# Optimization experiments

Hardware: AMD Instinct MI355X
Metric: run time of the kernel (lower is better)

Reference implementation:

```python
import jax, jax.numpy as jnp
import numpy as np

BS, SEQ, VOCAB, EMS, NHID, ML = 32, 512, 5000, 256, 512, 16
TEMP = 0.9
GAMMA = 0.0  # self.gamma is a fixed zero Variable in the original


def setup_inputs() -> dict:
    key = jax.random.key(0)
    ks = jax.random.split(key, 10)
    nm = SEQ // ML
    inputs = jax.random.randint(ks[0], (BS, SEQ), 0, VOCAB, dtype=jnp.int32)
    measure_steps = jax.random.randint(ks[1], (ML, BS, nm), 0, VOCAB, dtype=jnp.int32)
    measure_weights = jax.random.normal(ks[2], (BS, nm, nm), dtype=jnp.float32)
    h0 = jnp.zeros((BS, NHID), jnp.float32)
    c0 = jnp.zeros((BS, NHID), jnp.float32)
    initrange = 0.1
    emb = jax.random.uniform(ks[3], (VOCAB, EMS), minval=-initrange, maxval=initrange)
    k = 1.0 / np.sqrt(NHID).astype(np.float32)
    W_ih = jax.random.uniform(ks[4], (4 * NHID, EMS), minval=-k, maxval=k)
    W_hh = jax.random.uniform(ks[5], (4 * NHID, NHID), minval=-k, maxval=k)
    b_ih = jax.random.uniform(ks[6], (4 * NHID,), minval=-k, maxval=k)
    b_hh = jax.random.uniform(ks[7], (4 * NHID,), minval=-k, maxval=k)
    W_dec = jax.random.uniform(ks[8], (VOCAB, NHID), minval=-initrange, maxval=initrange)
    b_dec = jnp.zeros((VOCAB,), jnp.float32)
    return dict(inputs=inputs, h0=h0, c0=c0, measure_weights=measure_weights,
                measure_steps=measure_steps, emb=emb, W_ih=W_ih, W_hh=W_hh,
                b_ih=b_ih, b_hh=b_hh, W_dec=W_dec, b_dec=b_dec, measure_length=ML)


def _forward(h0, c0, mw, emb, W_ih, W_hh, b_ih, b_hh, W_dec, b_dec,
             inputs, msteps, measure_length):
    bs, seq = inputs.shape
    nm = seq // measure_length
    # attention over previous measures: softmax over j < m (causal-masked)
    mask = (jnp.arange(nm)[None, :] < jnp.arange(nm)[:, None]).astype(mw.dtype)  # [m, j]
    logits = jnp.where(mask[None] > 0, mw / TEMP, -1e9)
    sm = jax.nn.softmax(logits, axis=-1) * mask[None]  # [bs, m, j]
    prev_embs = emb[msteps]  # [ML, bs, nm, E]
    # lookback embedding for (measure m, step s): sum_j sm[b,m,j] * emb[steps[s,b,j]]
    lb = jnp.einsum('bmj,sbje->msbe', sm, prev_embs)  # [nm, ML, bs, E]
    lb_seq = lb.reshape(seq, bs, -1)  # time-major: t = m*ML + s
    # per-step bmm decode against embedding table: [bs, seq, V]
    lookback = jnp.einsum('tbe,ve->btv', lb_seq, emb)
    # original zeros lookback for timesteps with int(i/num_measures)==0, i.e. i < nm
    tmask = (jnp.arange(seq) >= nm)[None, :, None]
    lookback = jnp.where(tmask, lookback, jnp.zeros((), lookback.dtype))

    x = emb[inputs]  # [bs, seq, E] (single channel -> concat is identity)

    def cell(carry, xt):
        h, c = carry
        g = xt @ W_ih.T + b_ih + h @ W_hh.T + b_hh
        i, f, gg, o = jnp.split(g, 4, axis=-1)
        c2 = jax.nn.sigmoid(f) * c + jax.nn.sigmoid(i) * jnp.tanh(gg)
        h2 = jax.nn.sigmoid(o) * jnp.tanh(c2)
        return (h2, c2), h2

    (hT, cT), hs = jax.lax.scan(cell, (h0, c0), jnp.swapaxes(x, 0, 1))
    out = jnp.swapaxes(hs, 0, 1)  # [bs, seq, nhid]
    decoded = out @ W_dec.T + b_dec  # [bs, seq, V]
    dec = (1.0 - GAMMA) * decoded + GAMMA * lookback
    return dec, hT, cT


def reference(inputs, h0, c0, measure_weights, measure_steps, emb,
              W_ih, W_hh, b_ih, b_hh, W_dec, b_dec, measure_length):
    return _forward(h0, c0, measure_weights, emb, W_ih, W_hh, b_ih, b_hh,
                    W_dec, b_dec, inputs, measure_steps, measure_length)
```

## Files before the change

### kernel.cpp

```cpp
#include <hip/hip_runtime.h>
#include <cstdint>
#include <cstddef>

#define BS     32
#define SEQ    512
#define VOCAB  5000
#define EMS    256
#define NHID   512
#define GH     2048
#define NWG    32
#define SLICE  16
#define VPAD   5120

#define WS_FLAGS 0
#define WS_BIAS  1024
#define WS_WIH   (WS_BIAS + GH*4)
#define WS_WHH   (WS_WIH + GH*EMS*2)
#define WS_WDH   (WS_WHH + GH*NHID*2)
#define WS_WDL   (WS_WDH + VPAD*NHID*2)
#define WS_X     (WS_WDL + VPAD*NHID*2)
#define WS_HHI   (WS_X + SEQ*BS*EMS*2)
#define WS_HLO   (WS_HHI + BS*SEQ*NHID*2)
#define WS_HBUF  (WS_HLO + BS*SEQ*NHID*2)
#define WS_END   (WS_HBUF + 2*BS*NHID*2)

typedef float f32x4 __attribute__((ext_vector_type(4)));
typedef __bf16 bf16x8 __attribute__((ext_vector_type(8)));

static __device__ __forceinline__ uint16_t f2bf(float x) {
  uint32_t u = __builtin_bit_cast(uint32_t, x);
  u += 0x7FFFu + ((u >> 16) & 1u);
  return (uint16_t)(u >> 16);
}
static __device__ __forceinline__ float bf2f(uint16_t b) {
  return __builtin_bit_cast(float, (uint32_t)b << 16);
}
static __device__ __forceinline__ float sigf(float x) { return 1.0f / (1.0f + __expf(-x)); }
static __device__ __forceinline__ float tanhf_fast(float x) {
  return 1.0f - 2.0f / (__expf(2.0f * x) + 1.0f);
}
static __device__ __forceinline__ f32x4 mfma16(uint4 a, uint4 b, f32x4 c) {
  return __builtin_amdgcn_mfma_f32_16x16x32_bf16(
      __builtin_bit_cast(bf16x8, a), __builtin_bit_cast(bf16x8, b), c, 0, 0, 0);
}
static __device__ __forceinline__ void glds16(const void* g, void* l) {
  __builtin_amdgcn_global_load_lds((__attribute__((address_space(1))) void*)g,
                                   (__attribute__((address_space(3))) void*)l,
                                   16, 0, 0);
}
static __device__ __forceinline__ void coh_store_u32(uint32_t* p, uint32_t v) {
  __hip_atomic_store(p, v, __ATOMIC_RELAXED, __HIP_MEMORY_SCOPE_AGENT);
}

__global__ __launch_bounds__(256) void prep_kernel(
    const int* __restrict__ inputs, const float* __restrict__ h0,
    const float* __restrict__ emb, const float* __restrict__ Wih,
    const float* __restrict__ Whh, const float* __restrict__ bih,
    const float* __restrict__ bhh, const float* __restrict__ Wd,
    char* __restrict__ ws) {
  int gid = blockIdx.x * 256 + threadIdx.x;
  int gsz = gridDim.x * 256;
  uint16_t* wX  = (uint16_t*)(ws + WS_X);
  uint16_t* wIH = (uint16_t*)(ws + WS_WIH);
  uint16_t* wHH = (uint16_t*)(ws + WS_WHH);
  uint16_t* wDH = (uint16_t*)(ws + WS_WDH);
  uint16_t* wDL = (uint16_t*)(ws + WS_WDL);
  float*    bias = (float*)(ws + WS_BIAS);
  uint16_t* hb  = (uint16_t*)(ws + WS_HBUF);
  if (gid < 32) ((uint32_t*)(ws + WS_FLAGS))[gid] = 0u;
  for (int i = gid; i < SEQ*BS*EMS; i += gsz) {
    int e = i & (EMS-1), b = (i >> 8) & (BS-1), t = i >> 13;
    wX[i] = f2bf(emb[(size_t)inputs[b*SEQ + t] * EMS + e]);
  }
  for (int i = gid; i < GH*EMS; i += gsz)  wIH[i] = f2bf(Wih[i]);
  for (int i = gid; i < GH*NHID; i += gsz) wHH[i] = f2bf(Whh[i]);
  for (int i = gid; i < VPAD*NHID; i += gsz) {
    int row = i >> 9;
    uint16_t hi = 0, lo = 0;
    if (row < VOCAB) {
      float x = Wd[i];
      hi = f2bf(x);
      lo = f2bf(x - bf2f(hi));
    }
    wDH[i] = hi; wDL[i] = lo;
  }
  for (int i = gid; i < GH; i += gsz) bias[i] = bih[i] + bhh[i];
  for (int i = gid; i < BS*NHID; i += gsz) hb[i] = f2bf(h0[i]);
}

template <int KSTEPS, int NPASS>
__global__ __launch_bounds__(256) void gemm_kernel(
    const uint16_t* __restrict__ A0, const uint16_t* __restrict__ A1,
    const uint16_t* __restrict__ A2, const uint16_t* __restrict__ B0,
    const uint16_t* __restrict__ B1, const uint16_t* __restrict__ B2,
    const float* __restrict__ bias, float* __restrict__ out,
    int Nvalid, int ldout) {
  constexpr int K = KSTEPS * 32;
  constexpr int TOT = KSTEPS * NPASS;
  __shared__ __align__(16) char lds[4][8192];
  const int tid = threadIdx.x;
  const int lane = tid & 63, w = tid >> 6;
  const int m0 = blockIdx.y * 128, n0 = blockIdx.x * 128;
  const uint16_t* As[3] = {A0, A1, A2};
  const uint16_t* Bs[3] = {B0, B1, B2};
  const int wbase = (tid & ~63);

  auto stage = [&](int buf, int s) {
    const int p = s / KSTEPS, kk = s % KSTEPS;
    const uint16_t* A = As[p];
    const uint16_t* B = Bs[p];
    char* dA = &lds[buf*2][0];
    char* dB = &lds[buf*2+1][0];
#pragma unroll
    for (int c = 0; c < 2; ++c) {
      int idx = c*256 + tid;
      int row = idx >> 2, col = (idx & 3) * 8;
      glds16(A + (size_t)(m0 + row) * K + kk*32 + col, dA + (c*256 + wbase)*16);
      glds16(B + (size_t)(n0 + row) * K + kk*32 + col, dB + (c*256 + wbase)*16);
    }
  };

  const f32x4 zero = {0.f, 0.f, 0.f, 0.f};
  f32x4 acc[4][4];
#pragma unroll
  for (int i = 0; i < 4; ++i)
#pragma unroll
    for (int j = 0; j < 4; ++j) acc[i][j] = zero;

  const int mq = (w >> 1) * 64, nq = (w & 1) * 64;
  stage(0, 0);
  for (int s = 0; s < TOT; ++s) {
    __syncthreads();
    if (s + 1 < TOT) stage((s + 1) & 1, s + 1);
    const char* cA = &lds[(s & 1)*2][0];
    const char* cB = &lds[(s & 1)*2+1][0];
    uint4 a[4], b[4];
#pragma unroll
    for (int i = 0; i < 4; ++i) {
      a[i] = *(const uint4*)(cA + (mq + i*16 + (lane & 15))*64 + (lane >> 4)*16);
      b[i] = *(const uint4*)(cB + (nq + i*16 + (lane & 15))*64 + (lane >> 4)*16);
    }
#pragma unroll
    for (int i = 0; i < 4; ++i)
#pragma unroll
      for (int j = 0; j < 4; ++j) acc[i][j] = mfma16(a[i], b[j], acc[i][j]);
  }
#pragma unroll
  for (int j = 0; j < 4; ++j) {
    int V = n0 + nq + j*16 + (lane & 15);
    if (V >= Nvalid) continue;
    float bv = bias[V];
#pragma unroll
    for (int i = 0; i < 4; ++i) {
      int Rb = m0 + mq + i*16 + (lane >> 4)*4;
#pragma unroll
      for (int r = 0; r < 4; ++r)
        out[(size_t)(Rb + r) * ldout + V] = acc[i][j][r] + bv;
    }
  }
}

__global__ __launch_bounds__(256, 1) void scan_kernel(
    const float* __restrict__ Gin, char* __restrict__ ws,
    const float* __restrict__ c0, float* __restrict__ outT) {
  __shared__ __align__(16) char sW[64*1024];
  __shared__ __align__(16) char sH[32*1024];
  __shared__ float sG[4*BS*SLICE];
  const uint16_t* wHH = (const uint16_t*)(ws + WS_WHH);
  uint16_t* hbuf = (uint16_t*)(ws + WS_HBUF);
  uint16_t* Hhi  = (uint16_t*)(ws + WS_HHI);
  uint16_t* Hlo  = (uint16_t*)(ws + WS_HLO);
  uint32_t* flags = (uint32_t*)(ws + WS_FLAGS);
  const int tid = threadIdx.x, wg = blockIdx.x;
  const int lane = tid & 63, w = tid >> 6;
  const int mw = w >> 1, nw = w & 1;

  for (int c = tid; c < 4096; c += 256) {
    int row = c >> 6;
    int kb = (c & 63) * 16;
    int G = row >> 4, dl = row & 15;
    uint4 v = *(const uint4*)(wHH + (size_t)(G*NHID + wg*SLICE + dl) * NHID + kb/2);
    *(uint4*)(sW + row*1024 + (kb ^ ((row & 7) << 4))) = v;
  }
  const int bq = tid >> 3, dq = (tid & 7) * 2;
  float c_0 = c0[bq*NHID + wg*SLICE + dq];
  float c_1 = c0[bq*NHID + wg*SLICE + dq + 1];
  const int arow = mw*16 + (lane & 15);
  const int brow0 = (2*nw)*16 + (lane & 15);
  const int brow1 = brow0 + 16;
  const int kb0 = (lane >> 4) * 16;

  float ga0[4], ga1[4], gb0[4], gb1[4];
  {
    const float* grow = Gin + wg*SLICE + (lane & 15);
#pragma unroll
    for (int r = 0; r < 4; ++r) {
      int b = mw*16 + (lane >> 4)*4 + r;
      ga0[r] = grow[(size_t)b*GH + (2*nw+0)*NHID];
      ga1[r] = grow[(size_t)b*GH + (2*nw+1)*NHID];
    }
  }
  __syncthreads();

  for (int t = 0; t < SEQ; ++t) {
    if (t > 0) {
      const uint32_t tgt = (uint32_t)t;
      const int fl = lane & 31;
      while (true) {
        uint32_t v = __hip_atomic_load(flags + fl, __ATOMIC_RELAXED, __HIP_MEMORY_SCOPE_AGENT);
        if (__all((int)(v >= tgt))) break;
      }
    }

    if (t + 1 < SEQ) {
      const float* grow = Gin + (size_t)(t+1)*(BS*GH) + wg*SLICE + (lane & 15);
#pragma unroll
      for (int r = 0; r < 4; ++r) {
        int b = mw*16 + (lane >> 4)*4 + r;
        gb0[r] = grow[(size_t)b*GH + (2*nw+0)*NHID];
        gb1[r] = grow[(size_t)b*GH + (2*nw+1)*NHID];
      }
    }

    {
      const char* hsrc = (const char*)(hbuf + (t & 1) * (BS*NHID));
      const char* pb = hsrc + tid * 16;
      uint4 v0, v1, v2, v3, v4, v5, v6, v7;
      asm volatile("global_load_dwordx4 %0, %1, off sc0 sc1" : "=v"(v0) : "v"(pb));
      asm volatile("global_load_dwordx4 %0, %1, off sc0 sc1" : "=v"(v1) : "v"(pb + 4096));
      asm volatile("global_load_dwordx4 %0, %1, off sc0 sc1" : "=v"(v2) : "v"(pb + 8192));
      asm volatile("global_load_dwordx4 %0, %1, off sc0 sc1" : "=v"(v3) : "v"(pb + 12288));
      asm volatile("global_load_dwordx4 %0, %1, off sc0 sc1" : "=v"(v4) : "v"(pb + 16384));
      asm volatile("global_load_dwordx4 %0, %1, off sc0 sc1" : "=v"(v5) : "v"(pb + 20480));
      asm volatile("global_load_dwordx4 %0, %1, off sc0 sc1" : "=v"(v6) : "v"(pb + 24576));
      asm volatile("global_load_dwordx4 %0, %1, off sc0 sc1" : "=v"(v7) : "v"(pb + 28672));
      asm volatile("s_waitcnt vmcnt(0)" ::: "memory");
      __builtin_amdgcn_sched_barrier(0);
      const int kb = (tid & 63) * 16;
      const int ww = tid >> 6;
#define STW(J, VJ) *(uint4*)(sH + ((J)*4 + ww)*1024 + (kb ^ ((((J)&1)*4 + ww) << 4))) = VJ;
      STW(0, v0) STW(1, v1) STW(2, v2) STW(3, v3)
      STW(4, v4) STW(5, v5) STW(6, v6) STW(7, v7)
#undef STW
    }
    __syncthreads();

    f32x4 acc0, acc1;
#pragma unroll
    for (int r = 0; r < 4; ++r) { acc0[r] = ga0[r]; acc1[r] = ga1[r]; }
#pragma unroll
    for (int kt = 0; kt < 16; ++kt) {
      int kb = kt*64 + kb0;
      uint4 av = *(const uint4*)(sH + arow*1024 + (kb ^ ((arow & 7) << 4)));
      uint4 b0 = *(const uint4*)(sW + brow0*1024 + (kb ^ ((brow0 & 7) << 4)));
      uint4 b1 = *(const uint4*)(sW + brow1*1024 + (kb ^ ((brow1 & 7) << 4)));
      acc0 = mfma16(av, b0, acc0);
      acc1 = mfma16(av, b1, acc1);
    }
#pragma unroll
    for (int r = 0; r < 4; ++r) {
      int b = mw*16 + (lane >> 4)*4 + r;
      sG[((2*nw+0)*BS + b)*SLICE + (lane & 15)] = acc0[r];
      sG[((2*nw+1)*BS + b)*SLICE + (lane & 15)] = acc1[r];
    }
#pragma unroll
    for (int r = 0; r < 4; ++r) { ga0[r] = gb0[r]; ga1[r] = gb1[r]; }
    __syncthreads();

    float gi0 = sG[(0*BS + bq)*SLICE + dq], gi1 = sG[(0*BS + bq)*SLICE + dq + 1];
    float gf0 = sG[(1*BS + bq)*SLICE + dq], gf1 = sG[(1*BS + bq)*SLICE + dq + 1];
    float gg0 = sG[(2*BS + bq)*SLICE + dq], gg1 = sG[(2*BS + bq)*SLICE + dq + 1];
    float go0 = sG[(3*BS + bq)*SLICE + dq], go1 = sG[(3*BS + bq)*SLICE + dq + 1];
    c_0 = sigf(gf0)*c_0 + sigf(gi0)*tanhf_fast(gg0);
    c_1 = sigf(gf1)*c_1 + sigf(gi1)*tanhf_fast(gg1);
    float h_0 = sigf(go0)*tanhf_fast(c_0);
    float h_1 = sigf(go1)*tanhf_fast(c_1);

    uint16_t hh0 = f2bf(h_0), hh1 = f2bf(h_1);
    uint32_t hp = (uint32_t)hh0 | ((uint32_t)hh1 << 16);
    coh_store_u32((uint32_t*)(hbuf + ((t+1) & 1)*(BS*NHID)) +
                      ((bq*NHID + wg*SLICE + dq) >> 1), hp);
    size_t hoff = ((size_t)bq*SEQ + t)*NHID + wg*SLICE + dq;
    *(uint32_t*)(Hhi + hoff) = hp;
    uint32_t lp = (uint32_t)f2bf(h_0 - bf2f(hh0)) | ((uint32_t)f2bf(h_1 - bf2f(hh1)) << 16);
    *(uint32_t*)(Hlo + hoff) = lp;
    if (t == SEQ-1) {
      outT[bq*NHID + wg*SLICE + dq]     = h_0;
      outT[bq*NHID + wg*SLICE + dq + 1] = h_1;
      outT[BS*NHID + bq*NHID + wg*SLICE + dq]     = c_0;
      outT[BS*NHID + bq*NHID + wg*SLICE + dq + 1] = c_1;
    }

    __syncthreads();
    if (tid == 0)
      __hip_atomic_store(flags + wg, (uint32_t)(t + 1), __ATOMIC_RELAXED,
                         __HIP_MEMORY_SCOPE_AGENT);
  }
}

extern "C" void kernel_launch(void* const* d_in, const int* in_sizes, int n_in,
                              void* d_out, int out_size, void* d_ws, size_t ws_size,
                              hipStream_t stream) {
  (void)in_sizes; (void)n_in; (void)out_size; (void)ws_size;
  const int*   inputs = (const int*)  d_in[0];
  const float* h0     = (const float*)d_in[1];
  const float* c0     = (const float*)d_in[2];
  const float* emb    = (const float*)d_in[5];
  const float* Wih    = (const float*)d_in[6];
  const float* Whh    = (const float*)d_in[7];
  const float* bih    = (const float*)d_in[8];
  const float* bhh    = (const float*)d_in[9];
  const float* Wdec   = (const float*)d_in[10];
  const float* bdec   = (const float*)d_in[11];
  char* ws   = (char*)d_ws;
  float* out = (float*)d_out;
  float* Gin  = out;
  float* outT = out + (size_t)BS*SEQ*VOCAB;

  prep_kernel<<<512, 256, 0, stream>>>(inputs, h0, emb, Wih, Whh, bih, bhh, Wdec, ws);
  gemm_kernel<8,1><<<dim3(GH/128, (BS*SEQ)/128), 256, 0, stream>>>(
      (const uint16_t*)(ws + WS_X), (const uint16_t*)(ws + WS_X), (const uint16_t*)(ws + WS_X),
      (const uint16_t*)(ws + WS_WIH), (const uint16_t*)(ws + WS_WIH), (const uint16_t*)(ws + WS_WIH),
      (const float*)(ws + WS_BIAS), Gin, GH, GH);
  scan_kernel<<<NWG, 256, 0, stream>>>(Gin, ws, c0, outT);
  gemm_kernel<16,3><<<dim3(VPAD/128, (BS*SEQ)/128), 256, 0, stream>>>(
      (const uint16_t*)(ws + WS_HHI), (const uint16_t*)(ws + WS_HHI), (const uint16_t*)(ws + WS_HLO),
      (const uint16_t*)(ws + WS_WDH), (const uint16_t*)(ws + WS_WDL), (const uint16_t*)(ws + WS_WDH),
      bdec, out, VOCAB, VOCAB);
}
```

Before: 2.056 ms.

## Replace per-block flag barrier with step-tagged hidden-state words in scan

```diff
diff --git a/kernel.cpp b/kernel.cpp
--- a/kernel.cpp
+++ b/kernel.cpp
@@ -12,7 +12,6 @@
 #define SLICE  16
 #define VPAD   5120
 
-#define WS_FLAGS 0
 #define WS_BIAS  1024
 #define WS_WIH   (WS_BIAS + GH*4)
 #define WS_WHH   (WS_WIH + GH*EMS*2)
@@ -21,8 +20,8 @@
 #define WS_X     (WS_WDL + VPAD*NHID*2)
 #define WS_HHI   (WS_X + SEQ*BS*EMS*2)
 #define WS_HLO   (WS_HHI + BS*SEQ*NHID*2)
-#define WS_HBUF  (WS_HLO + BS*SEQ*NHID*2)
-#define WS_END   (WS_HBUF + 2*BS*NHID*2)
+#define WS_TAG   (WS_HLO + BS*SEQ*NHID*2)
+#define WS_END   (WS_TAG + 2*8192*8)
 
 typedef float f32x4 __attribute__((ext_vector_type(4)));
 typedef __bf16 bf16x8 __attribute__((ext_vector_type(8)));
@@ -47,9 +46,6 @@
   __builtin_amdgcn_global_load_lds((__attribute__((address_space(1))) void*)g,
                                    (__attribute__((address_space(3))) void*)l,
                                    16, 0, 0);
-}
-static __device__ __forceinline__ void coh_store_u32(uint32_t* p, uint32_t v) {
-  __hip_atomic_store(p, v, __ATOMIC_RELAXED, __HIP_MEMORY_SCOPE_AGENT);
 }
 
 __global__ __launch_bounds__(256) void prep_kernel(
@@ -66,8 +62,7 @@
   uint16_t* wDH = (uint16_t*)(ws + WS_WDH);
   uint16_t* wDL = (uint16_t*)(ws + WS_WDL);
   float*    bias = (float*)(ws + WS_BIAS);
-  uint16_t* hb  = (uint16_t*)(ws + WS_HBUF);
-  if (gid < 32) ((uint32_t*)(ws + WS_FLAGS))[gid] = 0u;
+  unsigned long long* Tg = (unsigned long long*)(ws + WS_TAG);
   for (int i = gid; i < SEQ*BS*EMS; i += gsz) {
     int e = i & (EMS-1), b = (i >> 8) & (BS-1), t = i >> 13;
     wX[i] = f2bf(emb[(size_t)inputs[b*SEQ + t] * EMS + e]);
@@ -85,7 +80,14 @@
     wDH[i] = hi; wDL[i] = lo;
   }
   for (int i = gid; i < GH; i += gsz) bias[i] = bih[i] + bhh[i];
-  for (int i = gid; i < BS*NHID; i += gsz) hb[i] = f2bf(h0[i]);
+  for (int u = gid; u < 8192; u += gsz) {
+    int tc = u >> 5, j = u & 31;
+    int b = tc & 31, d = (tc >> 5) * 64 + j * 2;
+    uint32_t pay = (uint32_t)f2bf(h0[b*NHID + d]) |
+                   ((uint32_t)f2bf(h0[b*NHID + d + 1]) << 16);
+    Tg[u] = (unsigned long long)pay;
+    Tg[8192 + u] = 0xFFFFFFFF00000000ull;
+  }
 }
 
 template <int KSTEPS, int NPASS>
@@ -167,10 +169,9 @@
   __shared__ __align__(16) char sH[32*1024];
   __shared__ float sG[4*BS*SLICE];
   const uint16_t* wHH = (const uint16_t*)(ws + WS_WHH);
-  uint16_t* hbuf = (uint16_t*)(ws + WS_HBUF);
+  unsigned long long* Tg = (unsigned long long*)(ws + WS_TAG);
   uint16_t* Hhi  = (uint16_t*)(ws + WS_HHI);
   uint16_t* Hlo  = (uint16_t*)(ws + WS_HLO);
-  uint32_t* flags = (uint32_t*)(ws + WS_FLAGS);
   const int tid = threadIdx.x, wg = blockIdx.x;
   const int lane = tid & 63, w = tid >> 6;
   const int mw = w >> 1, nw = w & 1;
@@ -189,6 +190,8 @@
   const int brow0 = (2*nw)*16 + (lane & 15);
   const int brow1 = brow0 + 16;
   const int kb0 = (lane >> 4) * 16;
+  const int dmy = wg*SLICE + dq;
+  const int uidx = ((dmy >> 6) * 32 + bq) * 32 + ((dmy & 63) >> 1);
 
   float ga0[4], ga1[4], gb0[4], gb1[4];
   {
@@ -203,15 +206,6 @@
   __syncthreads();
 
   for (int t = 0; t < SEQ; ++t) {
-    if (t > 0) {
-      const uint32_t tgt = (uint32_t)t;
-      const int fl = lane & 31;
-      while (true) {
-        uint32_t v = __hip_atomic_load(flags + fl, __ATOMIC_RELAXED, __HIP_MEMORY_SCOPE_AGENT);
-        if (__all((int)(v >= tgt))) break;
-      }
-    }
-
     if (t + 1 < SEQ) {
       const float* grow = Gin + (size_t)(t+1)*(BS*GH) + wg*SLICE + (lane & 15);
 #pragma unroll
@@ -223,24 +217,47 @@
     }
 
     {
-      const char* hsrc = (const char*)(hbuf + (t & 1) * (BS*NHID));
-      const char* pb = hsrc + tid * 16;
-      uint4 v0, v1, v2, v3, v4, v5, v6, v7;
-      asm volatile("global_load_dwordx4 %0, %1, off sc0 sc1" : "=v"(v0) : "v"(pb));
-      asm volatile("global_load_dwordx4 %0, %1, off sc0 sc1" : "=v"(v1) : "v"(pb + 4096));
-      asm volatile("global_load_dwordx4 %0, %1, off sc0 sc1" : "=v"(v2) : "v"(pb + 8192));
-      asm volatile("global_load_dwordx4 %0, %1, off sc0 sc1" : "=v"(v3) : "v"(pb + 12288));
-      asm volatile("global_load_dwordx4 %0, %1, off sc0 sc1" : "=v"(v4) : "v"(pb + 16384));
-      asm volatile("global_load_dwordx4 %0, %1, off sc0 sc1" : "=v"(v5) : "v"(pb + 20480));
-      asm volatile("global_load_dwordx4 %0, %1, off sc0 sc1" : "=v"(v6) : "v"(pb + 24576));
-      asm volatile("global_load_dwordx4 %0, %1, off sc0 sc1" : "=v"(v7) : "v"(pb + 28672));
-      asm volatile("s_waitcnt vmcnt(0)" ::: "memory");
-      __builtin_amdgcn_sched_barrier(0);
-      const int kb = (tid & 63) * 16;
-      const int ww = tid >> 6;
-#define STW(J, VJ) *(uint4*)(sH + ((J)*4 + ww)*1024 + (kb ^ ((((J)&1)*4 + ww) << 4))) = VJ;
-      STW(0, v0) STW(1, v1) STW(2, v2) STW(3, v3)
-      STW(4, v4) STW(5, v5) STW(6, v6) STW(7, v7)
+      const char* tb = (const char*)(Tg + (size_t)(t & 1) * 8192) + tid * 256;
+      const uint32_t tg = (uint32_t)t;
+#define QD(J) uint2 q##J;
+      QD(0) QD(1) QD(2) QD(3) QD(4) QD(5) QD(6) QD(7)
+      QD(8) QD(9) QD(10) QD(11) QD(12) QD(13) QD(14) QD(15)
+      QD(16) QD(17) QD(18) QD(19) QD(20) QD(21) QD(22) QD(23)
+      QD(24) QD(25) QD(26) QD(27) QD(28) QD(29) QD(30) QD(31)
+#undef QD
+      uint32_t tries = 0;
+      for (;;) {
+#define PQ(J, OFF) asm volatile("global_load_dwordx2 %0, %1, off offset:" OFF " sc0 sc1" \
+                                : "=v"(q##J) : "v"(tb));
+        PQ(0,"0")    PQ(1,"8")    PQ(2,"16")   PQ(3,"24")
+        PQ(4,"32")   PQ(5,"40")   PQ(6,"48")   PQ(7,"56")
+        PQ(8,"64")   PQ(9,"72")   PQ(10,"80")  PQ(11,"88")
+        PQ(12,"96")  PQ(13,"104") PQ(14,"112") PQ(15,"120")
+        PQ(16,"128") PQ(17,"136") PQ(18,"144") PQ(19,"152")
+        PQ(20,"160") PQ(21,"168") PQ(22,"176") PQ(23,"184")
+        PQ(24,"192") PQ(25,"200") PQ(26,"208") PQ(27,"216")
+        PQ(28,"224") PQ(29,"232") PQ(30,"240") PQ(31,"248")
+#undef PQ
+        asm volatile("s_waitcnt vmcnt(0)" ::: "memory");
+        __builtin_amdgcn_sched_barrier(0);
+        uint32_t bad =
+            (q0.y^tg)|(q1.y^tg)|(q2.y^tg)|(q3.y^tg)|(q4.y^tg)|(q5.y^tg)|(q6.y^tg)|(q7.y^tg)|
+            (q8.y^tg)|(q9.y^tg)|(q10.y^tg)|(q11.y^tg)|(q12.y^tg)|(q13.y^tg)|(q14.y^tg)|(q15.y^tg)|
+            (q16.y^tg)|(q17.y^tg)|(q18.y^tg)|(q19.y^tg)|(q20.y^tg)|(q21.y^tg)|(q22.y^tg)|(q23.y^tg)|
+            (q24.y^tg)|(q25.y^tg)|(q26.y^tg)|(q27.y^tg)|(q28.y^tg)|(q29.y^tg)|(q30.y^tg)|(q31.y^tg);
+        if (bad == 0) break;
+        if (++tries > (1u << 20)) break;
+      }
+      char* dst = sH + (tid & 31) * 1024;
+      const int cb = (tid >> 5) * 128;
+      const int sw = (tid & 7) << 4;
+      uint4 wv;
+#define STW(K, A, B, C, D) wv.x = A.x; wv.y = B.x; wv.z = C.x; wv.w = D.x; \
+      *(uint4*)(dst + ((cb + (K)*16) ^ sw)) = wv;
+      STW(0, q0, q1, q2, q3)     STW(1, q4, q5, q6, q7)
+      STW(2, q8, q9, q10, q11)   STW(3, q12, q13, q14, q15)
+      STW(4, q16, q17, q18, q19) STW(5, q20, q21, q22, q23)
+      STW(6, q24, q25, q26, q27) STW(7, q28, q29, q30, q31)
 #undef STW
     }
     __syncthreads();
@@ -278,8 +295,9 @@
 
     uint16_t hh0 = f2bf(h_0), hh1 = f2bf(h_1);
     uint32_t hp = (uint32_t)hh0 | ((uint32_t)hh1 << 16);
-    coh_store_u32((uint32_t*)(hbuf + ((t+1) & 1)*(BS*NHID)) +
-                      ((bq*NHID + wg*SLICE + dq) >> 1), hp);
+    __hip_atomic_store(Tg + (size_t)((t + 1) & 1) * 8192 + uidx,
+                       ((unsigned long long)(uint32_t)(t + 1) << 32) | (unsigned long long)hp,
+                       __ATOMIC_RELAXED, __HIP_MEMORY_SCOPE_AGENT);
     size_t hoff = ((size_t)bq*SEQ + t)*NHID + wg*SLICE + dq;
     *(uint32_t*)(Hhi + hoff) = hp;
     uint32_t lp = (uint32_t)f2bf(h_0 - bf2f(hh0)) | ((uint32_t)f2bf(h_1 - bf2f(hh1)) << 16);
@@ -290,11 +308,6 @@
       outT[BS*NHID + bq*NHID + wg*SLICE + dq]     = c_0;
       outT[BS*NHID + bq*NHID + wg*SLICE + dq + 1] = c_1;
     }
-
-    __syncthreads();
-    if (tid == 0)
-      __hip_atomic_store(flags + wg, (uint32_t)(t + 1), __ATOMIC_RELAXED,
-                         __HIP_MEMORY_SCOPE_AGENT);
   }
 }
 
```

Result: slower. 4.009 ms (+95.0%).

## Fuse input projection, LSTM scan and decoder GEMM into one persistent kernel

Applied to the files above, without the earlier changes.

```diff
diff --git a/kernel.cpp b/kernel.cpp
--- a/kernel.cpp
+++ b/kernel.cpp
@@ -11,9 +11,12 @@
 #define NWG    32
 #define SLICE  16
 #define VPAD   5120
+#define NBLK   256
+#define NDEC   (NBLK - NWG)
+#define NTILE  ((BS*SEQ/128) * (VPAD/128))
 
 #define WS_FLAGS 0
-#define WS_BIAS  1024
+#define WS_BIAS  2048
 #define WS_WIH   (WS_BIAS + GH*4)
 #define WS_WHH   (WS_WIH + GH*EMS*2)
 #define WS_WDH   (WS_WHH + GH*NHID*2)
@@ -67,7 +70,7 @@
   uint16_t* wDL = (uint16_t*)(ws + WS_WDL);
   float*    bias = (float*)(ws + WS_BIAS);
   uint16_t* hb  = (uint16_t*)(ws + WS_HBUF);
-  if (gid < 32) ((uint32_t*)(ws + WS_FLAGS))[gid] = 0u;
+  if (gid < 512) ((uint32_t*)(ws + WS_FLAGS))[gid] = 0u;
   for (int i = gid; i < SEQ*BS*EMS; i += gsz) {
     int e = i & (EMS-1), b = (i >> 8) & (BS-1), t = i >> 13;
     wX[i] = f2bf(emb[(size_t)inputs[b*SEQ + t] * EMS + e]);
@@ -88,213 +91,246 @@
   for (int i = gid; i < BS*NHID; i += gsz) hb[i] = f2bf(h0[i]);
 }
 
-template <int KSTEPS, int NPASS>
-__global__ __launch_bounds__(256) void gemm_kernel(
-    const uint16_t* __restrict__ A0, const uint16_t* __restrict__ A1,
-    const uint16_t* __restrict__ A2, const uint16_t* __restrict__ B0,
-    const uint16_t* __restrict__ B1, const uint16_t* __restrict__ B2,
-    const float* __restrict__ bias, float* __restrict__ out,
-    int Nvalid, int ldout) {
-  constexpr int K = KSTEPS * 32;
-  constexpr int TOT = KSTEPS * NPASS;
-  __shared__ __align__(16) char lds[4][8192];
+__global__ __launch_bounds__(256, 1) void fused_kernel(
+    char* __restrict__ ws, const float* __restrict__ c0,
+    const float* __restrict__ bdec, float* __restrict__ out,
+    float* __restrict__ outT) {
+  __shared__ __align__(16) char smem[104 * 1024];
+  uint32_t* flags = (uint32_t*)(ws + WS_FLAGS);
   const int tid = threadIdx.x;
   const int lane = tid & 63, w = tid >> 6;
-  const int m0 = blockIdx.y * 128, n0 = blockIdx.x * 128;
-  const uint16_t* As[3] = {A0, A1, A2};
-  const uint16_t* Bs[3] = {B0, B1, B2};
-  const int wbase = (tid & ~63);
-
-  auto stage = [&](int buf, int s) {
-    const int p = s / KSTEPS, kk = s % KSTEPS;
-    const uint16_t* A = As[p];
-    const uint16_t* B = Bs[p];
-    char* dA = &lds[buf*2][0];
-    char* dB = &lds[buf*2+1][0];
-#pragma unroll
-    for (int c = 0; c < 2; ++c) {
-      int idx = c*256 + tid;
-      int row = idx >> 2, col = (idx & 3) * 8;
-      glds16(A + (size_t)(m0 + row) * K + kk*32 + col, dA + (c*256 + wbase)*16);
-      glds16(B + (size_t)(n0 + row) * K + kk*32 + col, dB + (c*256 + wbase)*16);
+
+  if (blockIdx.x < NWG) {
+    char* sW = smem;
+    char* sH = smem + 64*1024;
+    float* sG = (float*)(smem + 96*1024);
+    const uint16_t* wHH = (const uint16_t*)(ws + WS_WHH);
+    const uint16_t* wIH = (const uint16_t*)(ws + WS_WIH);
+    const uint16_t* wX  = (const uint16_t*)(ws + WS_X);
+    const float* bias = (const float*)(ws + WS_BIAS);
+    uint16_t* hbuf = (uint16_t*)(ws + WS_HBUF);
+    uint16_t* Hhi  = (uint16_t*)(ws + WS_HHI);
+    uint16_t* Hlo  = (uint16_t*)(ws + WS_HLO);
+    const int wg = blockIdx.x;
+    const int mw = w >> 1, nw = w & 1;
+
+    for (int c = tid; c < 4096; c += 256) {
+      int row = c >> 6;
+      int kb = (c & 63) * 16;
+      int G = row >> 4, dl = row & 15;
+      uint4 v = *(const uint4*)(wHH + (size_t)(G*NHID + wg*SLICE + dl) * NHID + kb/2);
+      *(uint4*)(sW + row*1024 + (kb ^ ((row & 7) << 4))) = v;
     }
-  };
-
-  const f32x4 zero = {0.f, 0.f, 0.f, 0.f};
-  f32x4 acc[4][4];
-#pragma unroll
-  for (int i = 0; i < 4; ++i)
-#pragma unroll
-    for (int j = 0; j < 4; ++j) acc[i][j] = zero;
-
-  const int mq = (w >> 1) * 64, nq = (w & 1) * 64;
-  stage(0, 0);
-  for (int s = 0; s < TOT; ++s) {
+    const int bq = tid >> 3, dq = (tid & 7) * 2;
+    float c_0 = c0[bq*NHID + wg*SLICE + dq];
+    float c_1 = c0[bq*NHID + wg*SLICE + dq + 1];
+    const int arow = mw*16 + (lane & 15);
+    const int brow0 = (2*nw)*16 + (lane & 15);
+    const int brow1 = brow0 + 16;
+    const int kb0 = (lane >> 4) * 16;
+    const int kfrag = (lane >> 4) * 8;
+    const float bs0 = bias[(2*nw+0)*NHID + wg*SLICE + (lane & 15)];
+    const float bs1 = bias[(2*nw+1)*NHID + wg*SLICE + (lane & 15)];
+    uint4 wbf[2][8];
+#pragma unroll
+    for (int g = 0; g < 2; ++g)
+#pragma unroll
+      for (int k2 = 0; k2 < 8; ++k2)
+        wbf[g][k2] = *(const uint4*)(wIH +
+            (size_t)((2*nw+g)*NHID + wg*SLICE + (lane & 15)) * EMS + k2*32 + kfrag);
+    uint4 xa[8], xb[8];
+#pragma unroll
+    for (int k2 = 0; k2 < 8; ++k2)
+      xa[k2] = *(const uint4*)(wX + (size_t)arow * EMS + k2*32 + kfrag);
     __syncthreads();
-    if (s + 1 < TOT) stage((s + 1) & 1, s + 1);
-    const char* cA = &lds[(s & 1)*2][0];
-    const char* cB = &lds[(s & 1)*2+1][0];
-    uint4 a[4], b[4];
-#pragma unroll
-    for (int i = 0; i < 4; ++i) {
-      a[i] = *(const uint4*)(cA + (mq + i*16 + (lane & 15))*64 + (lane >> 4)*16);
-      b[i] = *(const uint4*)(cB + (nq + i*16 + (lane & 15))*64 + (lane >> 4)*16);
-    }
-#pragma unroll
-    for (int i = 0; i < 4; ++i)
-#pragma unroll
-      for (int j = 0; j < 4; ++j) acc[i][j] = mfma16(a[i], b[j], acc[i][j]);
-  }
-#pragma unroll
-  for (int j = 0; j < 4; ++j) {
-    int V = n0 + nq + j*16 + (lane & 15);
-    if (V >= Nvalid) continue;
-    float bv = bias[V];
-#pragma unroll
-    for (int i = 0; i < 4; ++i) {
-      int Rb = m0 + mq + i*16 + (lane >> 4)*4;
-#pragma unroll
-      for (int r = 0; r < 4; ++r)
-        out[(size_t)(Rb + r) * ldout + V] = acc[i][j][r] + bv;
-    }
-  }
-}
-
-__global__ __launch_bounds__(256, 1) void scan_kernel(
-    const float* __restrict__ Gin, char* __restrict__ ws,
-    const float* __restrict__ c0, float* __restrict__ outT) {
-  __shared__ __align__(16) char sW[64*1024];
-  __shared__ __align__(16) char sH[32*1024];
-  __shared__ float sG[4*BS*SLICE];
-  const uint16_t* wHH = (const uint16_t*)(ws + WS_WHH);
-  uint16_t* hbuf = (uint16_t*)(ws + WS_HBUF);
-  uint16_t* Hhi  = (uint16_t*)(ws + WS_HHI);
-  uint16_t* Hlo  = (uint16_t*)(ws + WS_HLO);
-  uint32_t* flags = (uint32_t*)(ws + WS_FLAGS);
-  const int tid = threadIdx.x, wg = blockIdx.x;
-  const int lane = tid & 63, w = tid >> 6;
-  const int mw = w >> 1, nw = w & 1;
-
-  for (int c = tid; c < 4096; c += 256) {
-    int row = c >> 6;
-    int kb = (c & 63) * 16;
-    int G = row >> 4, dl = row & 15;
-    uint4 v = *(const uint4*)(wHH + (size_t)(G*NHID + wg*SLICE + dl) * NHID + kb/2);
-    *(uint4*)(sW + row*1024 + (kb ^ ((row & 7) << 4))) = v;
-  }
-  const int bq = tid >> 3, dq = (tid & 7) * 2;
-  float c_0 = c0[bq*NHID + wg*SLICE + dq];
-  float c_1 = c0[bq*NHID + wg*SLICE + dq + 1];
-  const int arow = mw*16 + (lane & 15);
-  const int brow0 = (2*nw)*16 + (lane & 15);
-  const int brow1 = brow0 + 16;
-  const int kb0 = (lane >> 4) * 16;
-
-  float ga0[4], ga1[4], gb0[4], gb1[4];
-  {
-    const float* grow = Gin + wg*SLICE + (lane & 15);
-#pragma unroll
-    for (int r = 0; r < 4; ++r) {
-      int b = mw*16 + (lane >> 4)*4 + r;
-      ga0[r] = grow[(size_t)b*GH + (2*nw+0)*NHID];
-      ga1[r] = grow[(size_t)b*GH + (2*nw+1)*NHID];
-    }
-  }
-  __syncthreads();
-
-  for (int t = 0; t < SEQ; ++t) {
-    if (t > 0) {
-      const uint32_t tgt = (uint32_t)t;
-      const int fl = lane & 31;
-      while (true) {
-        uint32_t v = __hip_atomic_load(flags + fl, __ATOMIC_RELAXED, __HIP_MEMORY_SCOPE_AGENT);
-        if (__all((int)(v >= tgt))) break;
-      }
-    }
-
-    if (t + 1 < SEQ) {
-      const float* grow = Gin + (size_t)(t+1)*(BS*GH) + wg*SLICE + (lane & 15);
+
+    for (int t = 0; t < SEQ; ++t) {
+      if (t > 0) {
+        const uint32_t tgt = (uint32_t)t;
+        const uint32_t* fp = flags + (lane & 31) * 16;
+        uint32_t ptries = 0;
+        for (;;) {
+          uint32_t v = __hip_atomic_load(fp, __ATOMIC_RELAXED, __HIP_MEMORY_SCOPE_AGENT);
+          if (__all((int)(v >= tgt))) break;
+          if (++ptries > (1u << 20)) break;
+        }
+      }
+
+      uint4 v0, v1, v2, v3, v4, v5, v6, v7;
+      {
+        const char* pb = (const char*)(hbuf + (t & 1) * (BS*NHID)) + tid * 16;
+        asm volatile("global_load_dwordx4 %0, %1, off sc0 sc1" : "=v"(v0) : "v"(pb));
+        asm volatile("global_load_dwordx4 %0, %1, off sc0 sc1" : "=v"(v1) : "v"(pb + 4096));
+        asm volatile("global_load_dwordx4 %0, %1, off sc0 sc1" : "=v"(v2) : "v"(pb + 8192));
+        asm volatile("global_load_dwordx4 %0, %1, off sc0 sc1" : "=v"(v3) : "v"(pb + 12288));
+        asm volatile("global_load_dwordx4 %0, %1, off sc0 sc1" : "=v"(v4) : "v"(pb + 16384));
+        asm volatile("global_load_dwordx4 %0, %1, off sc0 sc1" : "=v"(v5) : "v"(pb + 20480));
+        asm volatile("global_load_dwordx4 %0, %1, off sc0 sc1" : "=v"(v6) : "v"(pb + 24576));
+        asm volatile("global_load_dwordx4 %0, %1, off sc0 sc1" : "=v"(v7) : "v"(pb + 28672));
+        const int tn = (t + 1 < SEQ) ? (t + 1) : 0;
+        const uint16_t* xp = wX + (size_t)(tn*BS + arow) * EMS + kfrag;
+        asm volatile("global_load_dwordx4 %0, %1, off"             : "=v"(xb[0]) : "v"(xp));
+        asm volatile("global_load_dwordx4 %0, %1, off offset:64"   : "=v"(xb[1]) : "v"(xp));
+        asm volatile("global_load_dwordx4 %0, %1, off offset:128"  : "=v"(xb[2]) : "v"(xp));
+        asm volatile("global_load_dwordx4 %0, %1, off offset:192"  : "=v"(xb[3]) : "v"(xp));
+        asm volatile("global_load_dwordx4 %0, %1, off offset:256"  : "=v"(xb[4]) : "v"(xp));
+        asm volatile("global_load_dwordx4 %0, %1, off offset:320"  : "=v"(xb[5]) : "v"(xp));
+        asm volatile("global_load_dwordx4 %0, %1, off offset:384"  : "=v"(xb[6]) : "v"(xp));
+        asm volatile("global_load_dwordx4 %0, %1, off offset:448"  : "=v"(xb[7]) : "v"(xp));
+      }
+      f32x4 acc0, acc1;
+#pragma unroll
+      for (int r = 0; r < 4; ++r) { acc0[r] = bs0; acc1[r] = bs1; }
+#pragma unroll
+      for (int k2 = 0; k2 < 8; ++k2) {
+        acc0 = mfma16(xa[k2], wbf[0][k2], acc0);
+        acc1 = mfma16(xa[k2], wbf[1][k2], acc1);
+      }
+      asm volatile("s_waitcnt vmcnt(8)" ::: "memory");
+      __builtin_amdgcn_sched_barrier(0);
+      {
+        const int kb = (tid & 63) * 16;
+        const int ww = tid >> 6;
+#define STW(J, VJ) *(uint4*)(sH + ((J)*4 + ww)*1024 + (kb ^ ((((J)&1)*4 + ww) << 4))) = VJ;
+        STW(0, v0) STW(1, v1) STW(2, v2) STW(3, v3)
+        STW(4, v4) STW(5, v5) STW(6, v6) STW(7, v7)
+#undef STW
+      }
+      __syncthreads();
+
+#pragma unroll
+      for (int kt = 0; kt < 16; ++kt) {
+        int kb = kt*64 + kb0;
+        uint4 av = *(const uint4*)(sH + arow*1024 + (kb ^ ((arow & 7) << 4)));
+        uint4 b0 = *(const uint4*)(sW + brow0*1024 + (kb ^ ((brow0 & 7) << 4)));
+        uint4 b1 = *(const uint4*)(sW + brow1*1024 + (kb ^ ((brow1 & 7) << 4)));
+        acc0 = mfma16(av, b0, acc0);
+        acc1 = mfma16(av, b1, acc1);
+      }
 #pragma unroll
       for (int r = 0; r < 4; ++r) {
         int b = mw*16 + (lane >> 4)*4 + r;
-        gb0[r] = grow[(size_t)b*GH + (2*nw+0)*NHID];
-        gb1[r] = grow[(size_t)b*GH + (2*nw+1)*NHID];
-      }
+        sG[((2*nw+0)*BS + b)*SLICE + (lane & 15)] = acc0[r];
+        sG[((2*nw+1)*BS + b)*SLICE + (lane & 15)] = acc1[r];
+      }
+#pragma unroll
+      for (int k2 = 0; k2 < 8; ++k2) xa[k2] = xb[k2];
+      __syncthreads();
+
+      float gi0 = sG[(0*BS + bq)*SLICE + dq], gi1 = sG[(0*BS + bq)*SLICE + dq + 1];
+      float gf0 = sG[(1*BS + bq)*SLICE + dq], gf1 = sG[(1*BS + bq)*SLICE + dq + 1];
+      float gg0 = sG[(2*BS + bq)*SLICE + dq], gg1 = sG[(2*BS + bq)*SLICE + dq + 1];
+      float go0 = sG[(3*BS + bq)*SLICE + dq], go1 = sG[(3*BS + bq)*SLICE + dq + 1];
+      c_0 = sigf(gf0)*c_0 + sigf(gi0)*tanhf_fast(gg0);
+      c_1 = sigf(gf1)*c_1 + sigf(gi1)*tanhf_fast(gg1);
+      float h_0 = sigf(go0)*tanhf_fast(c_0);
+      float h_1 = sigf(go1)*tanhf_fast(c_1);
+
+      uint16_t hh0 = f2bf(h_0), hh1 = f2bf(h_1);
+      uint32_t hp = (uint32_t)hh0 | ((uint32_t)hh1 << 16);
+      coh_store_u32((uint32_t*)(hbuf + ((t+1) & 1)*(BS*NHID)) +
+                        ((bq*NHID + wg*SLICE + dq) >> 1), hp);
+      size_t hoff = ((size_t)t*BS + bq)*NHID + wg*SLICE + dq;
+      coh_store_u32((uint32_t*)(Hhi + hoff), hp);
+      uint32_t lp = (uint32_t)f2bf(h_0 - bf2f(hh0)) | ((uint32_t)f2bf(h_1 - bf2f(hh1)) << 16);
+      coh_store_u32((uint32_t*)(Hlo + hoff), lp);
+      if (t == SEQ-1) {
+        outT[bq*NHID + wg*SLICE + dq]     = h_0;
+        outT[bq*NHID + wg*SLICE + dq + 1] = h_1;
+        outT[BS*NHID + bq*NHID + wg*SLICE + dq]     = c_0;
+        outT[BS*NHID + bq*NHID + wg*SLICE + dq + 1] = c_1;
+      }
+
+      __syncthreads();
+      if (tid == 0)
+        __hip_atomic_store(flags + wg * 16, (uint32_t)(t + 1),
+                           __ATOMIC_RELAXED, __HIP_MEMORY_SCOPE_AGENT);
     }
-
-    {
-      const char* hsrc = (const char*)(hbuf + (t & 1) * (BS*NHID));
-      const char* pb = hsrc + tid * 16;
-      uint4 v0, v1, v2, v3, v4, v5, v6, v7;
-      asm volatile("global_load_dwordx4 %0, %1, off sc0 sc1" : "=v"(v0) : "v"(pb));
-      asm volatile("global_load_dwordx4 %0, %1, off sc0 sc1" : "=v"(v1) : "v"(pb + 4096));
-      asm volatile("global_load_dwordx4 %0, %1, off sc0 sc1" : "=v"(v2) : "v"(pb + 8192));
-      asm volatile("global_load_dwordx4 %0, %1, off sc0 sc1" : "=v"(v3) : "v"(pb + 12288));
-      asm volatile("global_load_dwordx4 %0, %1, off sc0 sc1" : "=v"(v4) : "v"(pb + 16384));
-      asm volatile("global_load_dwordx4 %0, %1, off sc0 sc1" : "=v"(v5) : "v"(pb + 20480));
-      asm volatile("global_load_dwordx4 %0, %1, off sc0 sc1" : "=v"(v6) : "v"(pb + 24576));
-      asm volatile("global_load_dwordx4 %0, %1, off sc0 sc1" : "=v"(v7) : "v"(pb + 28672));
-      asm volatile("s_waitcnt vmcnt(0)" ::: "memory");
-      __builtin_amdgcn_sched_barrier(0);
-      const int kb = (tid & 63) * 16;
-      const int ww = tid >> 6;
-#define STW(J, VJ) *(uint4*)(sH + ((J)*4 + ww)*1024 + (kb ^ ((((J)&1)*4 + ww) << 4))) = VJ;
-      STW(0, v0) STW(1, v1) STW(2, v2) STW(3, v3)
-      STW(4, v4) STW(5, v5) STW(6, v6) STW(7, v7)
-#undef STW
+  } else {
+    char* lds = smem;
+    const uint16_t* Hhi = (const uint16_t*)(ws + WS_HHI);
+    const uint16_t* Hlo = (const uint16_t*)(ws + WS_HLO);
+    const uint16_t* WDH = (const uint16_t*)(ws + WS_WDH);
+    const uint16_t* WDL = (const uint16_t*)(ws + WS_WDL);
+    const uint16_t* As[3] = {Hhi, Hhi, Hlo};
+    const uint16_t* Bs[3] = {WDH, WDL, WDH};
+    const int widx = (int)blockIdx.x - NWG;
+    const int wbase = (tid & ~63);
+    const int mq = (w >> 1) * 64, nq = (w & 1) * 64;
+
+    for (int q = widx; q < NTILE; q += NDEC) {
+      const int mt = q / 40, nt = q % 40;
+      const int m0 = mt * 128, n0 = nt * 128;
+      if (w == 0) {
+        const uint32_t tgt = (uint32_t)(mt*4 + 4);
+        const uint32_t* fp = flags + (lane & 31) * 16;
+        uint32_t tries = 0;
+        for (;;) {
+          uint32_t v = __hip_atomic_load(fp, __ATOMIC_RELAXED, __HIP_MEMORY_SCOPE_AGENT);
+          if (__all((int)(v >= tgt))) break;
+          __builtin_amdgcn_s_sleep(16);
+          if (++tries > (1u << 15)) break;
+        }
+      }
+      __syncthreads();
+
+      auto stage = [&](int buf, int s) {
+        const int p = s >> 4, kk = s & 15;
+        const uint16_t* A = As[p];
+        const uint16_t* B = Bs[p];
+        char* dA = lds + buf*16384;
+        char* dB = lds + buf*16384 + 8192;
+#pragma unroll
+        for (int c2 = 0; c2 < 2; ++c2) {
+          int idx = c2*256 + tid;
+          int row = idx >> 2, col = (idx & 3) * 8;
+          glds16(A + (size_t)(m0 + row) * NHID + kk*32 + col, dA + (c2*256 + wbase)*16);
+          glds16(B + (size_t)(n0 + row) * NHID + kk*32 + col, dB + (c2*256 + wbase)*16);
+        }
+      };
+
+      const f32x4 zero = {0.f, 0.f, 0.f, 0.f};
+      f32x4 acc[4][4];
+#pragma unroll
+      for (int i = 0; i < 4; ++i)
+#pragma unroll
+        for (int j = 0; j < 4; ++j) acc[i][j] = zero;
+
+      stage(0, 0);
+      for (int s = 0; s < 48; ++s) {
+        __syncthreads();
+        if (s + 1 < 48) stage((s + 1) & 1, s + 1);
+        const char* cA = lds + (s & 1)*16384;
+        const char* cB = lds + (s & 1)*16384 + 8192;
+        uint4 a[4], b[4];
+#pragma unroll
+        for (int i = 0; i < 4; ++i) {
+          a[i] = *(const uint4*)(cA + (mq + i*16 + (lane & 15))*64 + (lane >> 4)*16);
+          b[i] = *(const uint4*)(cB + (nq + i*16 + (lane & 15))*64 + (lane >> 4)*16);
+        }
+#pragma unroll
+        for (int i = 0; i < 4; ++i)
+#pragma unroll
+          for (int j = 0; j < 4; ++j) acc[i][j] = mfma16(a[i], b[j], acc[i][j]);
+      }
+#pragma unroll
+      for (int j = 0; j < 4; ++j) {
+        int V = n0 + nq + j*16 + (lane & 15);
+        if (V >= VOCAB) continue;
+        float bv = bdec[V];
+#pragma unroll
+        for (int i = 0; i < 4; ++i) {
+          int Rb = m0 + mq + i*16 + (lane >> 4)*4;
+#pragma unroll
+          for (int r = 0; r < 4; ++r) {
+            int rr = Rb + r;
+            int orow = (rr & 31) * SEQ + (rr >> 5);
+            out[(size_t)orow * VOCAB + V] = acc[i][j][r] + bv;
+          }
+        }
+      }
+      __syncthreads();
     }
-    __syncthreads();
-
-    f32x4 acc0, acc1;
-#pragma unroll
-    for (int r = 0; r < 4; ++r) { acc0[r] = ga0[r]; acc1[r] = ga1[r]; }
-#pragma unroll
-    for (int kt = 0; kt < 16; ++kt) {
-      int kb = kt*64 + kb0;
-      uint4 av = *(const uint4*)(sH + arow*1024 + (kb ^ ((arow & 7) << 4)));
-      uint4 b0 = *(const uint4*)(sW + brow0*1024 + (kb ^ ((brow0 & 7) << 4)));
-      uint4 b1 = *(const uint4*)(sW + brow1*1024 + (kb ^ ((brow1 & 7) << 4)));
-      acc0 = mfma16(av, b0, acc0);
-      acc1 = mfma16(av, b1, acc1);
-    }
-#pragma unroll
-    for (int r = 0; r < 4; ++r) {
-      int b = mw*16 + (lane >> 4)*4 + r;
-      sG[((2*nw+0)*BS + b)*SLICE + (lane & 15)] = acc0[r];
-      sG[((2*nw+1)*BS + b)*SLICE + (lane & 15)] = acc1[r];
-    }
-#pragma unroll
-    for (int r = 0; r < 4; ++r) { ga0[r] = gb0[r]; ga1[r] = gb1[r]; }
-    __syncthreads();
-
-    float gi0 = sG[(0*BS + bq)*SLICE + dq], gi1 = sG[(0*BS + bq)*SLICE + dq + 1];
-    float gf0 = sG[(1*BS + bq)*SLICE + dq], gf1 = sG[(1*BS + bq)*SLICE + dq + 1];
-    float gg0 = sG[(2*BS + bq)*SLICE + dq], gg1 = sG[(2*BS + bq)*SLICE + dq + 1];
-    float go0 = sG[(3*BS + bq)*SLICE + dq], go1 = sG[(3*BS + bq)*SLICE + dq + 1];
-    c_0 = sigf(gf0)*c_0 + sigf(gi0)*tanhf_fast(gg0);
-    c_1 = sigf(gf1)*c_1 + sigf(gi1)*tanhf_fast(gg1);
-    float h_0 = sigf(go0)*tanhf_fast(c_0);
-    float h_1 = sigf(go1)*tanhf_fast(c_1);
-
-    uint16_t hh0 = f2bf(h_0), hh1 = f2bf(h_1);
-    uint32_t hp = (uint32_t)hh0 | ((uint32_t)hh1 << 16);
-    coh_store_u32((uint32_t*)(hbuf + ((t+1) & 1)*(BS*NHID)) +
-                      ((bq*NHID + wg*SLICE + dq) >> 1), hp);
-    size_t hoff = ((size_t)bq*SEQ + t)*NHID + wg*SLICE + dq;
-    *(uint32_t*)(Hhi + hoff) = hp;
-    uint32_t lp = (uint32_t)f2bf(h_0 - bf2f(hh0)) | ((uint32_t)f2bf(h_1 - bf2f(hh1)) << 16);
-    *(uint32_t*)(Hlo + hoff) = lp;
-    if (t == SEQ-1) {
-      outT[bq*NHID + wg*SLICE + dq]     = h_0;
-      outT[bq*NHID + wg*SLICE + dq + 1] = h_1;
-      outT[BS*NHID + bq*NHID + wg*SLICE + dq]     = c_0;
-      outT[BS*NHID + bq*NHID + wg*SLICE + dq + 1] = c_1;
-    }
-
-    __syncthreads();
-    if (tid == 0)
-      __hip_atomic_store(flags + wg, (uint32_t)(t + 1), __ATOMIC_RELAXED,
-                         __HIP_MEMORY_SCOPE_AGENT);
   }
 }
 
@@ -314,17 +350,8 @@
   const float* bdec   = (const float*)d_in[11];
   char* ws   = (char*)d_ws;
   float* out = (float*)d_out;
-  float* Gin  = out;
   float* outT = out + (size_t)BS*SEQ*VOCAB;
 
   prep_kernel<<<512, 256, 0, stream>>>(inputs, h0, emb, Wih, Whh, bih, bhh, Wdec, ws);
-  gemm_kernel<8,1><<<dim3(GH/128, (BS*SEQ)/128), 256, 0, stream>>>(
-      (const uint16_t*)(ws + WS_X), (const uint16_t*)(ws + WS_X), (const uint16_t*)(ws + WS_X),
-      (const uint16_t*)(ws + WS_WIH), (const uint16_t*)(ws + WS_WIH), (const uint16_t*)(ws + WS_WIH),
-      (const float*)(ws + WS_BIAS), Gin, GH, GH);
-  scan_kernel<<<NWG, 256, 0, stream>>>(Gin, ws, c0, outT);
-  gemm_kernel<16,3><<<dim3(VPAD/128, (BS*SEQ)/128), 256, 0, stream>>>(
-      (const uint16_t*)(ws + WS_HHI), (const uint16_t*)(ws + WS_HHI), (const uint16_t*)(ws + WS_HLO),
-      (const uint16_t*)(ws + WS_WDH), (const uint16_t*)(ws + WS_WDL), (const uint16_t*)(ws + WS_WDH),
-      bdec, out, VOCAB, VOCAB);
-}
+  fused_kernel<<<NBLK, 256, 0, stream>>>(ws, c0, bdec, out, outT);
+}
```

After: 2.102 ms. 2.2% more time.
